# Optimization experiments

Hardware: AMD Instinct MI355X
Metric: run time of the kernel (lower is better)

The kernel has to match this reference:

```python
import jax, jax.numpy as jnp
import numpy as np

ALPHA = 0.1
NUM_CLASSES = 10000
FEAT_DIM = 256
BATCH = 8192


def setup_inputs() -> dict:
    key = jax.random.key(0)
    k1, k2, k3 = jax.random.split(key, 3)
    feat = jax.random.normal(k1, (BATCH, FEAT_DIM), dtype=jnp.float32)
    label = jax.random.randint(k2, (BATCH,), 0, NUM_CLASSES, dtype=jnp.int64)
    # centers parameter, initialized ~ randn as in the torch constructor
    centers = jax.random.normal(k3, (NUM_CLASSES, FEAT_DIM), dtype=jnp.float32)
    return {"feat": feat, "label": label, "centers": centers}


def reference(feat, label, centers):
    B = feat.shape[0]
    # dist[b,c] = ||feat[b] - centers[c]||^2, computed in GEMM form:
    # ||f||^2 + ||c||^2 - 2 f.c  (same math as the broadcast diff^2 sum)
    f_sq = jnp.sum(feat * feat, axis=-1, keepdims=True)          # [B, 1]
    c_sq = jnp.sum(centers * centers, axis=-1)[None, :]          # [1, C]
    cross = jnp.einsum('bd,cd->bc', feat, centers)               # [B, C]
    dist = f_sq + c_sq - 2.0 * cross                             # [B, C]

    # one-hot margin scaling: y_onehot = alpha * onehot(label) + 1
    onehot = jax.nn.one_hot(label, NUM_CLASSES, dtype=dist.dtype)  # [B, C]
    margin_dist = dist * (onehot * ALPHA + 1.0)

    margin_logits = -0.5 * margin_dist
    logits = -0.5 * dist

    # likelihood: mean over batch of 0.5 * ||feat - centers[label]||^2
    cdiff = feat - centers[label]                                 # [B, D]
    likelihood = jnp.sum(cdiff * cdiff) / (2.0 * B)
    return (logits, margin_logits, likelihood)
```

## Files before the change

kernel.cpp:

```cpp
#include <hip/hip_runtime.h>
#include <hip/hip_bf16.h>


#define ALPHA_ 0.1f
constexpr int BATCH = 8192;
constexpr int NCLS  = 10000;
constexpr int FDIM  = 256;

typedef __attribute__((ext_vector_type(8))) short bf16x8;
typedef __attribute__((ext_vector_type(4))) float f32x4;

__device__ __forceinline__ unsigned short f2bf(float f) {
  unsigned int u = __float_as_uint(f);
  u += 0x7FFF + ((u >> 16) & 1);
  return (unsigned short)(u >> 16);
}

__global__ void prep_kernel(const float* __restrict__ feat,
                            const float* __restrict__ centers,
                            unsigned short* __restrict__ fbf,
                            unsigned short* __restrict__ cbf,
                            float* __restrict__ fsq,
                            float* __restrict__ csq) {
  int gw = (int)((blockIdx.x * blockDim.x + threadIdx.x) >> 6);
  int lane = threadIdx.x & 63;
  if (gw >= BATCH + NCLS) return;
  const float* src; unsigned short* dst; float* sq;
  if (gw < BATCH) {
    src = feat + (size_t)gw * FDIM; dst = fbf + (size_t)gw * FDIM; sq = fsq + gw;
  } else {
    int r = gw - BATCH;
    src = centers + (size_t)r * FDIM; dst = cbf + (size_t)r * FDIM; sq = csq + r;
  }
  float4 v = reinterpret_cast<const float4*>(src)[lane];
  ushort4 b;
  b.x = f2bf(v.x); b.y = f2bf(v.y); b.z = f2bf(v.z); b.w = f2bf(v.w);
  reinterpret_cast<ushort4*>(dst)[lane] = b;
  float s = v.x*v.x + v.y*v.y + v.z*v.z + v.w*v.w;
  #pragma unroll
  for (int off = 32; off >= 1; off >>= 1) s += __shfl_xor(s, off, 64);
  if (lane == 0) *sq = s;
}

#define BM 128
#define BN 128
#define BK 64

__global__ __launch_bounds__(512, 4)
void gemm_kernel(const unsigned short* __restrict__ fbf,
                 const unsigned short* __restrict__ cbf,
                 const float* __restrict__ fsq,
                 const float* __restrict__ csq,
                 const int* __restrict__ label,
                 float* __restrict__ out_logits,
                 float* __restrict__ out_margin) {
  __shared__ unsigned short As[2][BM * BK];
  __shared__ unsigned short Bs[2][BN * BK];

  const int NTN = (NCLS + BN - 1) / BN;
  const int NWG = (BATCH / BM) * NTN;

  int bid = blockIdx.x;
  int wg = (bid & 7) * (NWG >> 3) + (bid >> 3);
  int mt = wg / NTN;
  int nt = wg - mt * NTN;

  const int tid  = threadIdx.x;
  const int lane = tid & 63;
  const int wid  = tid >> 6;
  const int wr   = (wid >> 2) * 64;
  const int wc   = (wid & 3) * 32;

  f32x4 acc[4][2];
  #pragma unroll
  for (int i = 0; i < 4; i++)
    #pragma unroll
    for (int j = 0; j < 2; j++) acc[i][j] = (f32x4){0.f, 0.f, 0.f, 0.f};

  const int sr = tid >> 3;
  const int sc = tid & 7;
  const size_t a_base = (size_t)(mt * BM) * FDIM;
  const int c0 = nt * BN;

  bf16x8 va[2], vb[2];
  #define LOADT(kc_) do {                                                      \
    int k0 = (kc_) * BK;                                                       \
    _Pragma("unroll")                                                          \
    for (int j = 0; j < 2; ++j) {                                              \
      int r = j * 64 + sr;                                                     \
      va[j] = *reinterpret_cast<const bf16x8*>(fbf + a_base + (size_t)r * FDIM + k0 + sc * 8); \
      int cc = c0 + r; cc = (cc < NCLS) ? cc : (NCLS - 1);                     \
      vb[j] = *reinterpret_cast<const bf16x8*>(cbf + (size_t)cc * FDIM + k0 + sc * 8); \
    }                                                                          \
  } while (0)
  #define STORET(b_) do {                                                      \
    _Pragma("unroll")                                                          \
    for (int j = 0; j < 2; ++j) {                                              \
      int r = j * 64 + sr;                                                     \
      int off = r * BK + ((sc ^ (r & 7)) * 8);                                 \
      *reinterpret_cast<bf16x8*>(&As[b_][off]) = va[j];                        \
      *reinterpret_cast<bf16x8*>(&Bs[b_][off]) = vb[j];                        \
    }                                                                          \
  } while (0)

  LOADT(0);
  STORET(0);

  #pragma unroll
  for (int kc = 0; kc < FDIM / BK; ++kc) {
    const int cur = kc & 1;
    if (kc < FDIM / BK - 1) LOADT(kc + 1);
    __syncthreads();
    #pragma unroll
    for (int kk = 0; kk < BK / 32; ++kk) {
      const int ch = kk * 4 + (lane >> 4);
      bf16x8 a[4], b[2];
      #pragma unroll
      for (int i = 0; i < 4; i++) {
        int row = wr + i * 16 + (lane & 15);
        a[i] = *reinterpret_cast<const bf16x8*>(&As[cur][row * BK + ((ch ^ (row & 7)) * 8)]);
      }
      #pragma unroll
      for (int j = 0; j < 2; j++) {
        int row = wc + j * 16 + (lane & 15);
        b[j] = *reinterpret_cast<const bf16x8*>(&Bs[cur][row * BK + ((ch ^ (row & 7)) * 8)]);
      }
      #pragma unroll
      for (int i = 0; i < 4; i++)
        #pragma unroll
        for (int j = 0; j < 2; j++)
          acc[i][j] = __builtin_amdgcn_mfma_f32_16x16x32_bf16(b[j], a[i], acc[i][j], 0, 0, 0);
    }
    if (kc < FDIM / BK - 1) STORET(cur ^ 1);
  }

  const int mloc = wr + (lane & 15);
  const int nbase = wc + ((lane >> 4) << 2);
  #pragma unroll
  for (int i = 0; i < 4; i++) {
    int m = mt * BM + mloc + i * 16;
    float fs = fsq[m];
    int lb = label[m];
    size_t rowoff = (size_t)m * NCLS;
    #pragma unroll
    for (int j = 0; j < 2; j++) {
      int n0 = c0 + nbase + j * 16;
      if (n0 >= NCLS) continue;
      float4 cs = *reinterpret_cast<const float4*>(&csq[n0]);
      f32x4 v = acc[i][j];
      f32x4 lg;
      lg[0] = v[0] - 0.5f * (fs + cs.x);
      lg[1] = v[1] - 0.5f * (fs + cs.y);
      lg[2] = v[2] - 0.5f * (fs + cs.z);
      lg[3] = v[3] - 0.5f * (fs + cs.w);
      __builtin_nontemporal_store(lg, reinterpret_cast<f32x4*>(&out_logits[rowoff + n0]));
      f32x4 mg;
      mg[0] = (lb == n0    ) ? lg[0] * (1.0f + ALPHA_) : lg[0];
      mg[1] = (lb == n0 + 1) ? lg[1] * (1.0f + ALPHA_) : lg[1];
      mg[2] = (lb == n0 + 2) ? lg[2] * (1.0f + ALPHA_) : lg[2];
      mg[3] = (lb == n0 + 3) ? lg[3] * (1.0f + ALPHA_) : lg[3];
      __builtin_nontemporal_store(mg, reinterpret_cast<f32x4*>(&out_margin[rowoff + n0]));
    }
  }
  #undef LOADT
  #undef STORET
}

__global__ void lik_partial_kernel(const float* __restrict__ feat,
                                   const int* __restrict__ label,
                                   const float* __restrict__ centers,
                                   float* __restrict__ partial) {
  int t = threadIdx.x;
  int b0 = blockIdx.x * 8;
  float acc = 0.f;
  #pragma unroll
  for (int i = 0; i < 8; i++) {
    int row = b0 + i;
    int lb = label[row];
    float d = feat[(size_t)row * FDIM + t] - centers[(size_t)lb * FDIM + t];
    acc += d * d;
  }
  #pragma unroll
  for (int off = 32; off >= 1; off >>= 1) acc += __shfl_xor(acc, off, 64);
  __shared__ float red[4];
  if ((t & 63) == 0) red[t >> 6] = acc;
  __syncthreads();
  if (t == 0) partial[blockIdx.x] = red[0] + red[1] + red[2] + red[3];
}

__global__ void lik_final_kernel(const float* __restrict__ partial,
                                 float* __restrict__ out) {
  int t = threadIdx.x;
  float v = partial[t] + partial[t + 256] + partial[t + 512] + partial[t + 768];
  #pragma unroll
  for (int off = 32; off >= 1; off >>= 1) v += __shfl_xor(v, off, 64);
  __shared__ float red[4];
  if ((t & 63) == 0) red[t >> 6] = v;
  __syncthreads();
  if (t == 0) out[0] = (red[0] + red[1] + red[2] + red[3]) * (1.0f / (2.0f * BATCH));
}

extern "C" void kernel_launch(void* const* d_in, const int* in_sizes, int n_in,
                              void* d_out, int out_size, void* d_ws, size_t ws_size,
                              hipStream_t stream) {
  const float* feat    = (const float*)d_in[0];
  const int*   label   = (const int*)d_in[1];
  const float* centers = (const float*)d_in[2];

  float* out        = (float*)d_out;
  float* out_logits = out;
  float* out_margin = out + (size_t)BATCH * NCLS;
  float* out_lik    = out + 2 * (size_t)BATCH * NCLS;

  char* ws = (char*)d_ws;
  unsigned short* fbf = (unsigned short*)ws;
  unsigned short* cbf = (unsigned short*)(ws + (size_t)BATCH * FDIM * 2);
  float* fsq     = (float*)(ws + (size_t)BATCH * FDIM * 2 + (size_t)NCLS * FDIM * 2);
  float* csq     = fsq + BATCH;
  float* partial = csq + NCLS;

  prep_kernel<<<(BATCH + NCLS) / 4, 256, 0, stream>>>(feat, centers, fbf, cbf, fsq, csq);
  lik_partial_kernel<<<BATCH / 8, 256, 0, stream>>>(feat, label, centers, partial);
  lik_final_kernel<<<1, 256, 0, stream>>>(partial, out_lik);
  gemm_kernel<<<(BATCH / BM) * ((NCLS + BN - 1) / BN), 512, 0, stream>>>(
      fbf, cbf, fsq, csq, label, out_logits, out_margin);
}
```

Measured before the change: 210.7 us.

## Derive likelihood from GEMM logits at label column and use regular stores

Drops the separate likelihood kernel that re-read feat and gathered centers rows. Instead, the GEMM epilogue writes the negated logit at each row's label column, which equals half the squared distance, and a single 1024-thread kernel sums these per-row values. It also replaces the nontemporal output stores with ordinary vector stores. The fused likelihood now uses the bf16 GEMM result rather than fp32 differences, which adds precision error and cancellation from the norm-expansion form.

```diff
diff --git a/kernel.cpp b/kernel.cpp
--- a/kernel.cpp
+++ b/kernel.cpp
@@ -53,7 +53,8 @@
                  const float* __restrict__ csq,
                  const int* __restrict__ label,
                  float* __restrict__ out_logits,
-                 float* __restrict__ out_margin) {
+                 float* __restrict__ out_margin,
+                 float* __restrict__ lik_row) {
   __shared__ unsigned short As[2][BM * BK];
   __shared__ unsigned short Bs[2][BN * BK];
 
@@ -153,51 +154,40 @@
       lg[1] = v[1] - 0.5f * (fs + cs.y);
       lg[2] = v[2] - 0.5f * (fs + cs.z);
       lg[3] = v[3] - 0.5f * (fs + cs.w);
-      __builtin_nontemporal_store(lg, reinterpret_cast<f32x4*>(&out_logits[rowoff + n0]));
+      *reinterpret_cast<f32x4*>(&out_logits[rowoff + n0]) = lg;
       f32x4 mg;
       mg[0] = (lb == n0    ) ? lg[0] * (1.0f + ALPHA_) : lg[0];
       mg[1] = (lb == n0 + 1) ? lg[1] * (1.0f + ALPHA_) : lg[1];
       mg[2] = (lb == n0 + 2) ? lg[2] * (1.0f + ALPHA_) : lg[2];
       mg[3] = (lb == n0 + 3) ? lg[3] * (1.0f + ALPHA_) : lg[3];
-      __builtin_nontemporal_store(mg, reinterpret_cast<f32x4*>(&out_margin[rowoff + n0]));
+      *reinterpret_cast<f32x4*>(&out_margin[rowoff + n0]) = mg;
+      if (lb == n0)          lik_row[m] = -lg[0];
+      else if (lb == n0 + 1) lik_row[m] = -lg[1];
+      else if (lb == n0 + 2) lik_row[m] = -lg[2];
+      else if (lb == n0 + 3) lik_row[m] = -lg[3];
     }
   }
   #undef LOADT
   #undef STORET
 }
 
-__global__ void lik_partial_kernel(const float* __restrict__ feat,
-                                   const int* __restrict__ label,
-                                   const float* __restrict__ centers,
-                                   float* __restrict__ partial) {
+__global__ void lik_reduce_kernel(const float* __restrict__ lik_row,
+                                  float* __restrict__ out) {
   int t = threadIdx.x;
-  int b0 = blockIdx.x * 8;
-  float acc = 0.f;
-  #pragma unroll
-  for (int i = 0; i < 8; i++) {
-    int row = b0 + i;
-    int lb = label[row];
-    float d = feat[(size_t)row * FDIM + t] - centers[(size_t)lb * FDIM + t];
-    acc += d * d;
-  }
-  #pragma unroll
-  for (int off = 32; off >= 1; off >>= 1) acc += __shfl_xor(acc, off, 64);
-  __shared__ float red[4];
-  if ((t & 63) == 0) red[t >> 6] = acc;
-  __syncthreads();
-  if (t == 0) partial[blockIdx.x] = red[0] + red[1] + red[2] + red[3];
-}
-
-__global__ void lik_final_kernel(const float* __restrict__ partial,
-                                 float* __restrict__ out) {
-  int t = threadIdx.x;
-  float v = partial[t] + partial[t + 256] + partial[t + 512] + partial[t + 768];
+  float v = 0.f;
+  #pragma unroll
+  for (int i = 0; i < BATCH / 1024; i++) v += lik_row[t + i * 1024];
   #pragma unroll
   for (int off = 32; off >= 1; off >>= 1) v += __shfl_xor(v, off, 64);
-  __shared__ float red[4];
+  __shared__ float red[16];
   if ((t & 63) == 0) red[t >> 6] = v;
   __syncthreads();
-  if (t == 0) out[0] = (red[0] + red[1] + red[2] + red[3]) * (1.0f / (2.0f * BATCH));
+  if (t == 0) {
+    float s = 0.f;
+    #pragma unroll
+    for (int i = 0; i < 16; i++) s += red[i];
+    out[0] = s * (1.0f / BATCH);
+  }
 }
 
 extern "C" void kernel_launch(void* const* d_in, const int* in_sizes, int n_in,
@@ -217,11 +207,10 @@
   unsigned short* cbf = (unsigned short*)(ws + (size_t)BATCH * FDIM * 2);
   float* fsq     = (float*)(ws + (size_t)BATCH * FDIM * 2 + (size_t)NCLS * FDIM * 2);
   float* csq     = fsq + BATCH;
-  float* partial = csq + NCLS;
+  float* lik_row = csq + NCLS;
 
   prep_kernel<<<(BATCH + NCLS) / 4, 256, 0, stream>>>(feat, centers, fbf, cbf, fsq, csq);
-  lik_partial_kernel<<<BATCH / 8, 256, 0, stream>>>(feat, label, centers, partial);
-  lik_final_kernel<<<1, 256, 0, stream>>>(partial, out_lik);
   gemm_kernel<<<(BATCH / BM) * ((NCLS + BN - 1) / BN), 512, 0, stream>>>(
-      fbf, cbf, fsq, csq, label, out_logits, out_margin);
-}
+      fbf, cbf, fsq, csq, label, out_logits, out_margin, lik_row);
+  lik_reduce_kernel<<<1, 1024, 0, stream>>>(lik_row, out_lik);
+}
```

After: 200.2 us. 5.0% less time.
